# Performance work log

Hardware: AMD Instinct MI355X
Metric: run time of the kernel (lower is better)

The kernel has to match this reference:

```python
import jax, jax.numpy as jnp
import numpy as np

B, N, D = 4, 256, 256
NEG = -1e9


def setup_inputs() -> dict:
    key = jax.random.key(0)
    k = jax.random.split(key, 5)
    scale1 = 1.0 / np.sqrt(4 * D)
    scale2 = 1.0 / np.sqrt(D)
    return {
        "shared": jax.random.normal(k[0], (B, N, D), dtype=jnp.float32),
        "W1": jax.random.uniform(k[1], (4 * D, D), jnp.float32, -scale1, scale1),
        "b1": jax.random.uniform(k[2], (D,), jnp.float32, -scale1, scale1),
        "W2": jax.random.uniform(k[3], (D, 1), jnp.float32, -scale2, scale2),
        "b2": jax.random.uniform(k[4], (1,), jnp.float32, -scale2, scale2),
    }


def reference(shared, W1, b1, W2, b2):
    # Linear on concat([src, tgt, |src-tgt|, src*tgt]) == sum of per-block matmuls.
    Wa, Wb, Wc, Wd = W1[:D], W1[D:2 * D], W1[2 * D:3 * D], W1[3 * D:]
    src_t = jnp.einsum('bid,dh->bih', shared, Wa)        # [B,N,D]
    tgt_t = jnp.einsum('bjd,dh->bjh', shared, Wb)        # [B,N,D]
    diff = jnp.abs(shared[:, :, None, :] - shared[:, None, :, :])  # [B,N,N,D]
    prod = shared[:, :, None, :] * shared[:, None, :, :]           # [B,N,N,D]
    h = (src_t[:, :, None, :] + tgt_t[:, None, :, :]
         + jnp.einsum('bijd,dh->bijh', diff, Wc)
         + jnp.einsum('bijd,dh->bijh', prod, Wd) + b1)   # [B,N,N,D]
    h = jax.nn.silu(h)
    scores = jnp.einsum('bijh,h->bij', h, W2[:, 0]) + b2[0]  # [B,N,N]
    eye = jnp.eye(N, dtype=bool)[None]
    scores = jnp.where(eye, NEG, scores)
    return jax.nn.softmax(scores, axis=-1)
```

## Files before the change

kernel.cpp:

```cpp
#include <hip/hip_runtime.h>

#define BB 4
#define NN 256
#define DD 256
#define HH 256
#define NEGV -1.0e9f

typedef _Float16 half8 __attribute__((ext_vector_type(8)));
typedef __fp16   fp16x2 __attribute__((ext_vector_type(2)));
typedef float floatx4 __attribute__((ext_vector_type(4)));

__global__ __launch_bounds__(256) void prep_split(const float* __restrict__ X,
                                                  const float* __restrict__ W1,
                                                  float* __restrict__ S,
                                                  float* __restrict__ T,
                                                  _Float16* __restrict__ Wst) {
  const int g  = blockIdx.x;
  const int kk = blockIdx.y;
  const int h  = threadIdx.x;

  if (kk == 0 && g < 256) {
    const float wcv = W1[(size_t)(2 * DD + g) * HH + h];
    const float wdv = W1[(size_t)(3 * DD + g) * HH + h];
    const int ks = g >> 4;
    const int dd = g & 15;
    const int q  = dd >> 2;
    const int e  = (dd & 3) * 2;
    const int hgrp = h >> 4;
    const int ccw  = h & 15;
    _Float16* p = Wst + ((size_t)((ks * 16 + hgrp) * 4 + q) * 16 + ccw) * 8 + e;
    p[0] = (_Float16)wcv;
    p[1] = (_Float16)wdv;
  }

  const int row0 = g * 2;
  const int dbase = kk * 64;
  __shared__ float xr[2][64];
  if (h < 64)       xr[0][h]      = X[(size_t)row0 * DD + dbase + h];
  else if (h < 128) xr[1][h - 64] = X[(size_t)(row0 + 1) * DD + dbase + (h - 64)];
  __syncthreads();

  const float* __restrict__ Wa = W1 + (size_t)dbase * HH;
  const float* __restrict__ Wb = W1 + (size_t)(DD + dbase) * HH;
  float sa0 = 0.f, sa1 = 0.f, sb0 = 0.f, sb1 = 0.f;
#pragma unroll 8
  for (int d = 0; d < 64; ++d) {
    const float wa = Wa[(size_t)d * HH + h];
    const float wb = Wb[(size_t)d * HH + h];
    sa0 = fmaf(xr[0][d], wa, sa0);  sb0 = fmaf(xr[0][d], wb, sb0);
    sa1 = fmaf(xr[1][d], wa, sa1);  sb1 = fmaf(xr[1][d], wb, sb1);
  }
  atomicAdd(&S[(size_t)(row0 + 0) * HH + h], sa0);
  atomicAdd(&T[(size_t)(row0 + 0) * HH + h], sb0);
  atomicAdd(&S[(size_t)(row0 + 1) * HH + h], sa1);
  atomicAdd(&T[(size_t)(row0 + 1) * HH + h], sb1);
}

__device__ __forceinline__ half8 make_afrag(const float4 xi, const float4 xj) {
  fp16x2 p0 = __builtin_amdgcn_cvt_pkrtz(__builtin_fabsf(xi.x - xj.x), xi.x * xj.x);
  fp16x2 p1 = __builtin_amdgcn_cvt_pkrtz(__builtin_fabsf(xi.y - xj.y), xi.y * xj.y);
  fp16x2 p2 = __builtin_amdgcn_cvt_pkrtz(__builtin_fabsf(xi.z - xj.z), xi.z * xj.z);
  fp16x2 p3 = __builtin_amdgcn_cvt_pkrtz(__builtin_fabsf(xi.w - xj.w), xi.w * xj.w);
  uint4 u;
  u.x = __builtin_bit_cast(unsigned int, p0);
  u.y = __builtin_bit_cast(unsigned int, p1);
  u.z = __builtin_bit_cast(unsigned int, p2);
  u.w = __builtin_bit_cast(unsigned int, p3);
  return __builtin_bit_cast(half8, u);
}

#define MFMA16(af, bf, acc) acc = __builtin_amdgcn_mfma_f32_16x16x32_f16(af, bf, acc, 0, 0, 0)

__global__ __launch_bounds__(512, 4) void score_mfma(
    const float* __restrict__ X,  const float* __restrict__ b1,
    const float* __restrict__ W2, const float* __restrict__ b2,
    const float* __restrict__ S,  const float* __restrict__ T,
    const _Float16* __restrict__ Wst, float* __restrict__ Sc) {

  const int beta = blockIdx.x;
  const int b    = blockIdx.y;
  int i, qt;
  if (beta < 256)      { i = beta >> 2;                    qt = beta & 3; }
  else if (beta < 448) { const int g = beta - 256; const int d3 = g / 3;
                         i = 64 + d3;                      qt = 1 + (g - 3 * d3); }
  else if (beta < 576) { const int g = beta - 448;
                         i = 128 + (g >> 1);               qt = 2 + (g & 1); }
  else                 { i = 192 + (beta - 576);           qt = 3; }
  const int bi    = b * NN + i;
  const int jbase = qt * 64;
  const int isUp  = qt > (i >> 6);

  const int t     = threadIdx.x;
  const int lane  = t & 63;
  const int hg    = t >> 6;
  const int q     = lane >> 4;
  const int cc    = lane & 15;

  __shared__ __align__(16) float    xi_s[DD];
  __shared__ __align__(16) _Float16 Af[32768];
  __shared__ float pre_s[HH];
  __shared__ float pre2_s[HH];
  __shared__ float w2_s[HH];
  __shared__ float sc_s[8][64];

  if (t < 256) {
    xi_s[t]  = X[(size_t)bi * DD + t];
    pre_s[t] = S[(size_t)bi * HH + t] + b1[t];
  } else {
    const int u = t - 256;
    pre2_s[u] = T[(size_t)bi * HH + u] + b1[u];
    w2_s[u]   = W2[u];
  }

  const float* __restrict__ Tb = T + (size_t)b * NN * HH;
  const float* __restrict__ Sb = S + (size_t)b * NN * HH;

  const int jloc = t & 63;
  const int jg   = jloc >> 4;
  const int ccw  = jloc & 15;
  const float* __restrict__ xjrow = X + (size_t)(b * NN + jbase + jloc) * DD;

  const char* __restrict__ bsrc = (const char*)Wst + hg * 2048 + (size_t)lane * 16;

  __syncthreads();

  {
    const int sgrp = t >> 6;
#pragma unroll
    for (int idx = 0; idx < 8; ++idx) {
      const int ksqg = sgrp * 8 + idx;
      const int d0   = ksqg * 4;
      const int kg   = ksqg >> 2;
      const int qw   = ksqg & 3;
      const float4 xi4 = *(const float4*)&xi_s[d0];
      const float4 xj4 = *(const float4*)(xjrow + d0);
      *(half8*)&Af[kg * 2048 + (jg * 4 + qw) * 128 + ccw * 8] = make_afrag(xi4, xj4);
    }
  }
  __syncthreads();

  floatx4 acc0[4], acc1[4];
#pragma unroll
  for (int u = 0; u < 4; ++u) { acc0[u] = (floatx4)0.f; acc1[u] = (floatx4)0.f; }

  half8 Bf0[2], Bf1[2];
#pragma unroll
  for (int u = 0; u < 2; ++u) {
    Bf0[u] = *(const half8*)(bsrc + (size_t)u * 16384);
    Bf1[u] = *(const half8*)(bsrc + (size_t)u * 16384 + 1024);
  }
  const _Float16* ap0 = &Af[lane * 8];
  half8 An0 = *(const half8*)(ap0);
  half8 An1 = *(const half8*)(ap0 + 512);
  half8 An2 = *(const half8*)(ap0 + 1024);
  half8 An3 = *(const half8*)(ap0 + 1536);

#pragma unroll
  for (int kg = 0; kg < 16; ++kg) {
    const int s = kg & 1;
    const half8 Bc0 = Bf0[s], Bc1 = Bf1[s];
    const half8 Ac0 = An0, Ac1 = An1, Ac2 = An2, Ac3 = An3;
    if (kg < 14) {
      const char* bk = bsrc + (size_t)(kg + 2) * 16384;
      Bf0[s] = *(const half8*)(bk);
      Bf1[s] = *(const half8*)(bk + 1024);
    }
    if (kg < 15) {
      const _Float16* ap = &Af[(kg + 1) * 2048 + lane * 8];
      An0 = *(const half8*)(ap);
      An1 = *(const half8*)(ap + 512);
      An2 = *(const half8*)(ap + 1024);
      An3 = *(const half8*)(ap + 1536);
    }
    MFMA16(Ac0, Bc0, acc0[0]); MFMA16(Ac0, Bc1, acc1[0]);
    MFMA16(Ac1, Bc0, acc0[1]); MFMA16(Ac1, Bc1, acc1[1]);
    MFMA16(Ac2, Bc0, acc0[2]); MFMA16(Ac2, Bc1, acc1[2]);
    MFMA16(Ac3, Bc0, acc0[3]); MFMA16(Ac3, Bc1, acc1[3]);
  }

  const int h0   = hg * 32 + cc;
  const int h1   = h0 + 16;
  const int jrow = jbase + q * 4;

#define EPILOGUE(VROW, PRE) {                                                   \
    float tv0[16], tv1[16];                                                     \
    _Pragma("unroll")                                                           \
    for (int u = 0; u < 16; ++u) {                                              \
      const size_t j = (size_t)(jrow + (u >> 2) * 16 + (u & 3)) * HH;           \
      tv0[u] = VROW[j + h0];                                                    \
      tv1[u] = VROW[j + h1];                                                    \
    }                                                                           \
    const float w20 = w2_s[h0], pv0 = PRE[h0];                                  \
    const float w21 = w2_s[h1], pv1 = PRE[h1];                                  \
    float p[16];                                                                \
    _Pragma("unroll")                                                           \
    for (int u = 0; u < 16; ++u) {                                              \
      const float hv0 = acc0[u >> 2][u & 3] + pv0 + tv0[u];                     \
      const float sv0 = hv0 * __builtin_amdgcn_rcpf(1.f + __expf(-hv0));        \
      p[u] = sv0 * w20;                                                         \
      const float hv1 = acc1[u >> 2][u & 3] + pv1 + tv1[u];                     \
      const float sv1 = hv1 * __builtin_amdgcn_rcpf(1.f + __expf(-hv1));        \
      p[u] = fmaf(sv1, w21, p[u]);                                              \
    }                                                                           \
    _Pragma("unroll")                                                           \
    for (int u = 0; u < 16; ++u) {                                              \
      float v = p[u];                                                           \
      v += __shfl_xor(v, 1); v += __shfl_xor(v, 2);                             \
      v += __shfl_xor(v, 4); v += __shfl_xor(v, 8);                             \
      if (cc == 0) sc_s[hg][(u >> 2) * 16 + q * 4 + (u & 3)] = v;               \
    } }

  EPILOGUE(Tb, pre_s)
  __syncthreads();

  if (t < 64) {
    float s = sc_s[0][t] + sc_s[1][t] + sc_s[2][t] + sc_s[3][t]
            + sc_s[4][t] + sc_s[5][t] + sc_s[6][t] + sc_s[7][t] + b2[0];
    const int jg2 = jbase + t;
    if (jg2 == i) s = NEGV;
    Sc[(size_t)bi * NN + jg2] = s;
  }

  if (isUp) {
    __syncthreads();
    EPILOGUE(Sb, pre2_s)
    __syncthreads();
    if (t < 64) {
      const float s = sc_s[0][t] + sc_s[1][t] + sc_s[2][t] + sc_s[3][t]
                    + sc_s[4][t] + sc_s[5][t] + sc_s[6][t] + sc_s[7][t] + b2[0];
      Sc[(size_t)(b * NN + jbase + t) * NN + i] = s;
    }
  }
#undef EPILOGUE
}

__global__ __launch_bounds__(256) void softmax_kernel(const float* __restrict__ Sc,
                                                      float* __restrict__ out) {
  const int w    = threadIdx.x >> 6;
  const int lane = threadIdx.x & 63;
  const int bi   = blockIdx.x * 4 + w;
  const float4 v = *(const float4*)&Sc[(size_t)bi * NN + lane * 4];
  float m = fmaxf(fmaxf(v.x, v.y), fmaxf(v.z, v.w));
  m = fmaxf(m, __shfl_xor(m, 1));  m = fmaxf(m, __shfl_xor(m, 2));
  m = fmaxf(m, __shfl_xor(m, 4));  m = fmaxf(m, __shfl_xor(m, 8));
  m = fmaxf(m, __shfl_xor(m, 16)); m = fmaxf(m, __shfl_xor(m, 32));
  const float e0 = __expf(v.x - m), e1 = __expf(v.y - m);
  const float e2 = __expf(v.z - m), e3 = __expf(v.w - m);
  float sum = (e0 + e1) + (e2 + e3);
  sum += __shfl_xor(sum, 1);  sum += __shfl_xor(sum, 2);
  sum += __shfl_xor(sum, 4);  sum += __shfl_xor(sum, 8);
  sum += __shfl_xor(sum, 16); sum += __shfl_xor(sum, 32);
  const float r = 1.f / sum;
  float4 o; o.x = e0 * r; o.y = e1 * r; o.z = e2 * r; o.w = e3 * r;
  *(float4*)&out[(size_t)bi * NN + lane * 4] = o;
}

extern "C" void kernel_launch(void* const* d_in, const int* in_sizes, int n_in,
                              void* d_out, int out_size, void* d_ws, size_t ws_size,
                              hipStream_t stream) {
  const float* X  = (const float*)d_in[0];
  const float* W1 = (const float*)d_in[1];
  const float* b1 = (const float*)d_in[2];
  const float* W2 = (const float*)d_in[3];
  const float* b2 = (const float*)d_in[4];
  float* out = (float*)d_out;

  float*     Sws = (float*)d_ws;
  float*     Tws = Sws + (size_t)BB * NN * HH;
  _Float16*  Wst = (_Float16*)(Tws + (size_t)BB * NN * HH);
  float*     Scw = (float*)(Wst + (size_t)16 * HH * 32);

  hipMemsetAsync(Sws, 0, (size_t)2 * BB * NN * HH * sizeof(float), stream);

  prep_split<<<dim3(512, 4), 256, 0, stream>>>(X, W1, Sws, Tws, Wst);
  score_mfma<<<dim3(640, BB), 512, 0, stream>>>(X, b1, W2, b2, Sws, Tws, Wst, Scw);
  softmax_kernel<<<BB * NN / 4, 256, 0, stream>>>(Scw, out);
}
```

Baseline: 166.0 us.

## Process two query rows per block and drop atomic split-K in prep

The score kernel now handles two i rows per block, so each W-fragment global load feeds twice as many MFMAs and the xj row load is shared between both rows. The block count is halved, occupancy is lowered to 2 blocks per CU, and the A-fragment build is split into two k-halves to fit LDS. The prep kernel no longer splits K with atomics: each block does full 4-row dot products with float2 loads, which removes the memset and the atomic traffic. The cost is more registers (four accumulator sets), fewer resident waves, and an extra barrier pair per half.

```diff
diff --git a/kernel.cpp b/kernel.cpp
--- a/kernel.cpp
+++ b/kernel.cpp
@@ -10,50 +10,59 @@
 typedef __fp16   fp16x2 __attribute__((ext_vector_type(2)));
 typedef float floatx4 __attribute__((ext_vector_type(4)));
 
-__global__ __launch_bounds__(256) void prep_split(const float* __restrict__ X,
-                                                  const float* __restrict__ W1,
-                                                  float* __restrict__ S,
-                                                  float* __restrict__ T,
-                                                  _Float16* __restrict__ Wst) {
-  const int g  = blockIdx.x;
-  const int kk = blockIdx.y;
-  const int h  = threadIdx.x;
-
-  if (kk == 0 && g < 256) {
-    const float wcv = W1[(size_t)(2 * DD + g) * HH + h];
-    const float wdv = W1[(size_t)(3 * DD + g) * HH + h];
+__global__ __launch_bounds__(256) void prep(const float* __restrict__ X,
+                                            const float* __restrict__ W1,
+                                            float* __restrict__ S,
+                                            float* __restrict__ T,
+                                            _Float16* __restrict__ Wst) {
+  const int g = blockIdx.x;
+  const int t = threadIdx.x;
+
+  {
+    const float wcv = W1[(size_t)(2 * DD + g) * HH + t];
+    const float wdv = W1[(size_t)(3 * DD + g) * HH + t];
     const int ks = g >> 4;
     const int dd = g & 15;
     const int q  = dd >> 2;
     const int e  = (dd & 3) * 2;
-    const int hgrp = h >> 4;
-    const int ccw  = h & 15;
+    const int hgrp = t >> 4;
+    const int ccw  = t & 15;
     _Float16* p = Wst + ((size_t)((ks * 16 + hgrp) * 4 + q) * 16 + ccw) * 8 + e;
     p[0] = (_Float16)wcv;
     p[1] = (_Float16)wdv;
   }
 
-  const int row0 = g * 2;
-  const int dbase = kk * 64;
-  __shared__ float xr[2][64];
-  if (h < 64)       xr[0][h]      = X[(size_t)row0 * DD + dbase + h];
-  else if (h < 128) xr[1][h - 64] = X[(size_t)(row0 + 1) * DD + dbase + (h - 64)];
+  const int row0 = g * 4;
+  __shared__ float xr[4][256];
+  {
+    const float2* src2 = (const float2*)(X + (size_t)row0 * DD);
+    float2* xr2 = (float2*)xr;
+    xr2[t]       = src2[t];
+    xr2[t + 256] = src2[t + 256];
+  }
   __syncthreads();
 
-  const float* __restrict__ Wa = W1 + (size_t)dbase * HH;
-  const float* __restrict__ Wb = W1 + (size_t)(DD + dbase) * HH;
-  float sa0 = 0.f, sa1 = 0.f, sb0 = 0.f, sb1 = 0.f;
-#pragma unroll 8
-  for (int d = 0; d < 64; ++d) {
-    const float wa = Wa[(size_t)d * HH + h];
-    const float wb = Wb[(size_t)d * HH + h];
-    sa0 = fmaf(xr[0][d], wa, sa0);  sb0 = fmaf(xr[0][d], wb, sb0);
-    sa1 = fmaf(xr[1][d], wa, sa1);  sb1 = fmaf(xr[1][d], wb, sb1);
-  }
-  atomicAdd(&S[(size_t)(row0 + 0) * HH + h], sa0);
-  atomicAdd(&T[(size_t)(row0 + 0) * HH + h], sb0);
-  atomicAdd(&S[(size_t)(row0 + 1) * HH + h], sa1);
-  atomicAdd(&T[(size_t)(row0 + 1) * HH + h], sb1);
+  const int r2 = t >> 7;
+  const int h  = (t & 127) * 2;
+  const float* __restrict__ xA = xr[r2 * 2];
+  const float* __restrict__ xB = xr[r2 * 2 + 1];
+  float saAx = 0.f, saAy = 0.f, sbAx = 0.f, sbAy = 0.f;
+  float saBx = 0.f, saBy = 0.f, sbBx = 0.f, sbBy = 0.f;
+#pragma unroll 16
+  for (int d = 0; d < 256; ++d) {
+    const float2 wa = *(const float2*)&W1[(size_t)d * HH + h];
+    const float2 wb = *(const float2*)&W1[(size_t)(DD + d) * HH + h];
+    const float a = xA[d], c = xB[d];
+    saAx = fmaf(a, wa.x, saAx); saAy = fmaf(a, wa.y, saAy);
+    sbAx = fmaf(a, wb.x, sbAx); sbAy = fmaf(a, wb.y, sbAy);
+    saBx = fmaf(c, wa.x, saBx); saBy = fmaf(c, wa.y, saBy);
+    sbBx = fmaf(c, wb.x, sbBx); sbBy = fmaf(c, wb.y, sbBy);
+  }
+  const int rA = row0 + r2 * 2, rB = rA + 1;
+  *(float2*)&S[(size_t)rA * HH + h] = make_float2(saAx, saAy);
+  *(float2*)&S[(size_t)rB * HH + h] = make_float2(saBx, saBy);
+  *(float2*)&T[(size_t)rA * HH + h] = make_float2(sbAx, sbAy);
+  *(float2*)&T[(size_t)rB * HH + h] = make_float2(sbBx, sbBy);
 }
 
 __device__ __forceinline__ half8 make_afrag(const float4 xi, const float4 xj) {
@@ -71,7 +80,7 @@
 
 #define MFMA16(af, bf, acc) acc = __builtin_amdgcn_mfma_f32_16x16x32_f16(af, bf, acc, 0, 0, 0)
 
-__global__ __launch_bounds__(512, 4) void score_mfma(
+__global__ __launch_bounds__(512, 2) void score_mfma(
     const float* __restrict__ X,  const float* __restrict__ b1,
     const float* __restrict__ W2, const float* __restrict__ b2,
     const float* __restrict__ S,  const float* __restrict__ T,
@@ -79,16 +88,17 @@
 
   const int beta = blockIdx.x;
   const int b    = blockIdx.y;
-  int i, qt;
-  if (beta < 256)      { i = beta >> 2;                    qt = beta & 3; }
-  else if (beta < 448) { const int g = beta - 256; const int d3 = g / 3;
-                         i = 64 + d3;                      qt = 1 + (g - 3 * d3); }
-  else if (beta < 576) { const int g = beta - 448;
-                         i = 128 + (g >> 1);               qt = 2 + (g & 1); }
-  else                 { i = 192 + (beta - 576);           qt = 3; }
-  const int bi    = b * NN + i;
+  int m, qt;
+  if (beta < 128)      { m = beta >> 2;                    qt = beta & 3; }
+  else if (beta < 224) { const int g = beta - 128; const int d3 = g / 3;
+                         m = 32 + d3;                      qt = 1 + (g - 3 * d3); }
+  else if (beta < 288) { const int g = beta - 224;
+                         m = 64 + (g >> 1);                qt = 2 + (g & 1); }
+  else                 { m = 96 + (beta - 288);            qt = 3; }
+  const int i0    = m * 2;
+  const int bi0   = b * NN + i0;
   const int jbase = qt * 64;
-  const int isUp  = qt > (i >> 6);
+  const int isUp  = qt > (m >> 5);
 
   const int t     = threadIdx.x;
   const int lane  = t & 63;
@@ -96,20 +106,19 @@
   const int q     = lane >> 4;
   const int cc    = lane & 15;
 
-  __shared__ __align__(16) float    xi_s[DD];
-  __shared__ __align__(16) _Float16 Af[32768];
-  __shared__ float pre_s[HH];
-  __shared__ float pre2_s[HH];
+  __shared__ __align__(16) float    xi_s[2][DD];
+  __shared__ __align__(16) _Float16 Af[2][16384];
+  __shared__ float pre_s[2][HH];
+  __shared__ float pre2_s[2][HH];
   __shared__ float w2_s[HH];
-  __shared__ float sc_s[8][64];
-
-  if (t < 256) {
-    xi_s[t]  = X[(size_t)bi * DD + t];
-    pre_s[t] = S[(size_t)bi * HH + t] + b1[t];
-  } else {
-    const int u = t - 256;
-    pre2_s[u] = T[(size_t)bi * HH + u] + b1[u];
-    w2_s[u]   = W2[u];
+  __shared__ float sc_s[2][8][64];
+
+  {
+    const int ii = t >> 8, u = t & 255;
+    xi_s[ii][u]   = X[(size_t)(bi0 + ii) * DD + u];
+    pre_s[ii][u]  = S[(size_t)(bi0 + ii) * HH + u] + b1[u];
+    pre2_s[ii][u] = T[(size_t)(bi0 + ii) * HH + u] + b1[u];
+    if (t < 256) w2_s[t] = W2[t];
   }
 
   const float* __restrict__ Tb = T + (size_t)b * NN * HH;
@@ -122,26 +131,12 @@
 
   const char* __restrict__ bsrc = (const char*)Wst + hg * 2048 + (size_t)lane * 16;
 
-  __syncthreads();
-
-  {
-    const int sgrp = t >> 6;
+  floatx4 acc00[4], acc01[4], acc10[4], acc11[4];
 #pragma unroll
-    for (int idx = 0; idx < 8; ++idx) {
-      const int ksqg = sgrp * 8 + idx;
-      const int d0   = ksqg * 4;
-      const int kg   = ksqg >> 2;
-      const int qw   = ksqg & 3;
-      const float4 xi4 = *(const float4*)&xi_s[d0];
-      const float4 xj4 = *(const float4*)(xjrow + d0);
-      *(half8*)&Af[kg * 2048 + (jg * 4 + qw) * 128 + ccw * 8] = make_afrag(xi4, xj4);
-    }
-  }
-  __syncthreads();
-
-  floatx4 acc0[4], acc1[4];
-#pragma unroll
-  for (int u = 0; u < 4; ++u) { acc0[u] = (floatx4)0.f; acc1[u] = (floatx4)0.f; }
+  for (int u = 0; u < 4; ++u) {
+    acc00[u] = (floatx4)0.f; acc01[u] = (floatx4)0.f;
+    acc10[u] = (floatx4)0.f; acc11[u] = (floatx4)0.f;
+  }
 
   half8 Bf0[2], Bf1[2];
 #pragma unroll
@@ -149,33 +144,53 @@
     Bf0[u] = *(const half8*)(bsrc + (size_t)u * 16384);
     Bf1[u] = *(const half8*)(bsrc + (size_t)u * 16384 + 1024);
   }
-  const _Float16* ap0 = &Af[lane * 8];
-  half8 An0 = *(const half8*)(ap0);
-  half8 An1 = *(const half8*)(ap0 + 512);
-  half8 An2 = *(const half8*)(ap0 + 1024);
-  half8 An3 = *(const half8*)(ap0 + 1536);
+
+#pragma unroll 1
+  for (int half = 0; half < 2; ++half) {
+    __syncthreads();
 
 #pragma unroll
-  for (int kg = 0; kg < 16; ++kg) {
-    const int s = kg & 1;
-    const half8 Bc0 = Bf0[s], Bc1 = Bf1[s];
-    const half8 Ac0 = An0, Ac1 = An1, Ac2 = An2, Ac3 = An3;
-    if (kg < 14) {
-      const char* bk = bsrc + (size_t)(kg + 2) * 16384;
-      Bf0[s] = *(const half8*)(bk);
-      Bf1[s] = *(const half8*)(bk + 1024);
+    for (int idx = 0; idx < 4; ++idx) {
+      const int ksq = hg * 4 + idx;
+      const int d0  = (half * 32 + ksq) * 4;
+      const float4 xj4 = *(const float4*)(xjrow + d0);
+      const float4 xa4 = *(const float4*)&xi_s[0][d0];
+      const float4 xb4 = *(const float4*)&xi_s[1][d0];
+      const int off = (hg * 16 + jg * 4 + idx) * 128 + ccw * 8;
+      *(half8*)&Af[0][off] = make_afrag(xa4, xj4);
+      *(half8*)&Af[1][off] = make_afrag(xb4, xj4);
     }
-    if (kg < 15) {
-      const _Float16* ap = &Af[(kg + 1) * 2048 + lane * 8];
-      An0 = *(const half8*)(ap);
-      An1 = *(const half8*)(ap + 512);
-      An2 = *(const half8*)(ap + 1024);
-      An3 = *(const half8*)(ap + 1536);
+    __syncthreads();
+
+#pragma unroll
+    for (int ksl = 0; ksl < 8; ++ksl) {
+      const int s = ksl & 1;
+      const half8 Bc0 = Bf0[s], Bc1 = Bf1[s];
+      {
+        const int kn = (half * 8 + ksl + 2) & 15;
+        const char* bk = bsrc + (size_t)kn * 16384;
+        Bf0[s] = *(const half8*)(bk);
+        Bf1[s] = *(const half8*)(bk + 1024);
+      }
+      const _Float16* apA = &Af[0][ksl * 2048 + lane * 8];
+      const _Float16* apB = &Af[1][ksl * 2048 + lane * 8];
+      const half8 A00 = *(const half8*)(apA);
+      const half8 A01 = *(const half8*)(apA + 512);
+      const half8 A02 = *(const half8*)(apA + 1024);
+      const half8 A03 = *(const half8*)(apA + 1536);
+      const half8 A10 = *(const half8*)(apB);
+      const half8 A11 = *(const half8*)(apB + 512);
+      const half8 A12 = *(const half8*)(apB + 1024);
+      const half8 A13 = *(const half8*)(apB + 1536);
+      MFMA16(A00, Bc0, acc00[0]); MFMA16(A00, Bc1, acc01[0]);
+      MFMA16(A01, Bc0, acc00[1]); MFMA16(A01, Bc1, acc01[1]);
+      MFMA16(A02, Bc0, acc00[2]); MFMA16(A02, Bc1, acc01[2]);
+      MFMA16(A03, Bc0, acc00[3]); MFMA16(A03, Bc1, acc01[3]);
+      MFMA16(A10, Bc0, acc10[0]); MFMA16(A10, Bc1, acc11[0]);
+      MFMA16(A11, Bc0, acc10[1]); MFMA16(A11, Bc1, acc11[1]);
+      MFMA16(A12, Bc0, acc10[2]); MFMA16(A12, Bc1, acc11[2]);
+      MFMA16(A13, Bc0, acc10[3]); MFMA16(A13, Bc1, acc11[3]);
     }
-    MFMA16(Ac0, Bc0, acc0[0]); MFMA16(Ac0, Bc1, acc1[0]);
-    MFMA16(Ac1, Bc0, acc0[1]); MFMA16(Ac1, Bc1, acc1[1]);
-    MFMA16(Ac2, Bc0, acc0[2]); MFMA16(Ac2, Bc1, acc1[2]);
-    MFMA16(Ac3, Bc0, acc0[3]); MFMA16(Ac3, Bc1, acc1[3]);
   }
 
   const int h0   = hg * 32 + cc;
@@ -186,49 +201,66 @@
     float tv0[16], tv1[16];                                                     \
     _Pragma("unroll")                                                           \
     for (int u = 0; u < 16; ++u) {                                              \
-      const size_t j = (size_t)(jrow + (u >> 2) * 16 + (u & 3)) * HH;           \
-      tv0[u] = VROW[j + h0];                                                    \
-      tv1[u] = VROW[j + h1];                                                    \
+      const size_t jb = (size_t)(jrow + (u >> 2) * 16 + (u & 3)) * HH;          \
+      tv0[u] = VROW[jb + h0];                                                   \
+      tv1[u] = VROW[jb + h1];                                                   \
     }                                                                           \
-    const float w20 = w2_s[h0], pv0 = PRE[h0];                                  \
-    const float w21 = w2_s[h1], pv1 = PRE[h1];                                  \
-    float p[16];                                                                \
+    const float w20 = w2_s[h0], w21 = w2_s[h1];                                 \
+    const float pA0 = PRE[0][h0], pA1 = PRE[0][h1];                             \
+    const float pB0 = PRE[1][h0], pB1 = PRE[1][h1];                             \
+    float pI[16], pJ[16];                                                       \
     _Pragma("unroll")                                                           \
     for (int u = 0; u < 16; ++u) {                                              \
-      const float hv0 = acc0[u >> 2][u & 3] + pv0 + tv0[u];                     \
-      const float sv0 = hv0 * __builtin_amdgcn_rcpf(1.f + __expf(-hv0));        \
-      p[u] = sv0 * w20;                                                         \
-      const float hv1 = acc1[u >> 2][u & 3] + pv1 + tv1[u];                     \
-      const float sv1 = hv1 * __builtin_amdgcn_rcpf(1.f + __expf(-hv1));        \
-      p[u] = fmaf(sv1, w21, p[u]);                                              \
+      float hv, sv;                                                             \
+      hv = acc00[u >> 2][u & 3] + pA0 + tv0[u];                                 \
+      sv = hv * __builtin_amdgcn_rcpf(1.f + __expf(-hv));                       \
+      pI[u] = sv * w20;                                                         \
+      hv = acc01[u >> 2][u & 3] + pA1 + tv1[u];                                 \
+      sv = hv * __builtin_amdgcn_rcpf(1.f + __expf(-hv));                       \
+      pI[u] = fmaf(sv, w21, pI[u]);                                             \
+      hv = acc10[u >> 2][u & 3] + pB0 + tv0[u];                                 \
+      sv = hv * __builtin_amdgcn_rcpf(1.f + __expf(-hv));                       \
+      pJ[u] = sv * w20;                                                         \
+      hv = acc11[u >> 2][u & 3] + pB1 + tv1[u];                                 \
+      sv = hv * __builtin_amdgcn_rcpf(1.f + __expf(-hv));                       \
+      pJ[u] = fmaf(sv, w21, pJ[u]);                                             \
     }                                                                           \
     _Pragma("unroll")                                                           \
     for (int u = 0; u < 16; ++u) {                                              \
-      float v = p[u];                                                           \
+      float v = pI[u];                                                          \
       v += __shfl_xor(v, 1); v += __shfl_xor(v, 2);                             \
       v += __shfl_xor(v, 4); v += __shfl_xor(v, 8);                             \
-      if (cc == 0) sc_s[hg][(u >> 2) * 16 + q * 4 + (u & 3)] = v;               \
+      if (cc == 0) sc_s[0][hg][(u >> 2) * 16 + q * 4 + (u & 3)] = v;            \
+      float w = pJ[u];                                                          \
+      w += __shfl_xor(w, 1); w += __shfl_xor(w, 2);                             \
+      w += __shfl_xor(w, 4); w += __shfl_xor(w, 8);                             \
+      if (cc == 0) sc_s[1][hg][(u >> 2) * 16 + q * 4 + (u & 3)] = w;            \
     } }
 
   EPILOGUE(Tb, pre_s)
   __syncthreads();
 
-  if (t < 64) {
-    float s = sc_s[0][t] + sc_s[1][t] + sc_s[2][t] + sc_s[3][t]
-            + sc_s[4][t] + sc_s[5][t] + sc_s[6][t] + sc_s[7][t] + b2[0];
-    const int jg2 = jbase + t;
-    if (jg2 == i) s = NEGV;
-    Sc[(size_t)bi * NN + jg2] = s;
+  if (t < 128) {
+    const int r = t >> 6, jj = t & 63;
+    float s = sc_s[r][0][jj] + sc_s[r][1][jj] + sc_s[r][2][jj] + sc_s[r][3][jj]
+            + sc_s[r][4][jj] + sc_s[r][5][jj] + sc_s[r][6][jj] + sc_s[r][7][jj]
+            + b2[0];
+    const int jg2 = jbase + jj;
+    const int ii  = i0 + r;
+    if (jg2 == ii) s = NEGV;
+    Sc[(size_t)(b * NN + ii) * NN + jg2] = s;
   }
 
   if (isUp) {
     __syncthreads();
     EPILOGUE(Sb, pre2_s)
     __syncthreads();
-    if (t < 64) {
-      const float s = sc_s[0][t] + sc_s[1][t] + sc_s[2][t] + sc_s[3][t]
-                    + sc_s[4][t] + sc_s[5][t] + sc_s[6][t] + sc_s[7][t] + b2[0];
-      Sc[(size_t)(b * NN + jbase + t) * NN + i] = s;
+    if (t < 128) {
+      const int r = t >> 6, jj = t & 63;
+      const float s = sc_s[r][0][jj] + sc_s[r][1][jj] + sc_s[r][2][jj] + sc_s[r][3][jj]
+                    + sc_s[r][4][jj] + sc_s[r][5][jj] + sc_s[r][6][jj] + sc_s[r][7][jj]
+                    + b2[0];
+      Sc[(size_t)(b * NN + jbase + jj) * NN + (i0 + r)] = s;
     }
   }
 #undef EPILOGUE
@@ -270,9 +302,7 @@
   _Float16*  Wst = (_Float16*)(Tws + (size_t)BB * NN * HH);
   float*     Scw = (float*)(Wst + (size_t)16 * HH * 32);
 
-  hipMemsetAsync(Sws, 0, (size_t)2 * BB * NN * HH * sizeof(float), stream);
-
-  prep_split<<<dim3(512, 4), 256, 0, stream>>>(X, W1, Sws, Tws, Wst);
-  score_mfma<<<dim3(640, BB), 512, 0, stream>>>(X, b1, W2, b2, Sws, Tws, Wst, Scw);
+  prep<<<256, 256, 0, stream>>>(X, W1, Sws, Tws, Wst);
+  score_mfma<<<dim3(320, BB), 512, 0, stream>>>(X, b1, W2, b2, Sws, Tws, Wst, Scw);
   softmax_kernel<<<BB * NN / 4, 256, 0, stream>>>(Scw, out);
 }
```

After: 196.5 us. 1.18x slower.

## Drop split-K atomics in prep, deepen B prefetch, reorder score block mapping

Applied to the files above, without the earlier changes.

The prep kernel now computes each S/T row over the full D range with plain stores, which removes the memset and the atomicAdd split-K, and processes four rows per block with float2 weight loads. The score kernel's B-fragment prefetch goes from a depth of two to four and is issued before the A-fragment build barrier. The block index to (i, tile) mapping is regrouped by column tile. The gains are fewer launches and less atomic traffic plus more latency hiding, at the cost of fewer prep blocks and more registers in the score kernel.

```diff
diff --git a/kernel.cpp b/kernel.cpp
--- a/kernel.cpp
+++ b/kernel.cpp
@@ -10,50 +10,59 @@
 typedef __fp16   fp16x2 __attribute__((ext_vector_type(2)));
 typedef float floatx4 __attribute__((ext_vector_type(4)));
 
-__global__ __launch_bounds__(256) void prep_split(const float* __restrict__ X,
-                                                  const float* __restrict__ W1,
-                                                  float* __restrict__ S,
-                                                  float* __restrict__ T,
-                                                  _Float16* __restrict__ Wst) {
-  const int g  = blockIdx.x;
-  const int kk = blockIdx.y;
-  const int h  = threadIdx.x;
-
-  if (kk == 0 && g < 256) {
-    const float wcv = W1[(size_t)(2 * DD + g) * HH + h];
-    const float wdv = W1[(size_t)(3 * DD + g) * HH + h];
+__global__ __launch_bounds__(256) void prep(const float* __restrict__ X,
+                                            const float* __restrict__ W1,
+                                            float* __restrict__ S,
+                                            float* __restrict__ T,
+                                            _Float16* __restrict__ Wst) {
+  const int g = blockIdx.x;
+  const int t = threadIdx.x;
+
+  {
+    const float wcv = W1[(size_t)(2 * DD + g) * HH + t];
+    const float wdv = W1[(size_t)(3 * DD + g) * HH + t];
     const int ks = g >> 4;
     const int dd = g & 15;
     const int q  = dd >> 2;
     const int e  = (dd & 3) * 2;
-    const int hgrp = h >> 4;
-    const int ccw  = h & 15;
+    const int hgrp = t >> 4;
+    const int ccw  = t & 15;
     _Float16* p = Wst + ((size_t)((ks * 16 + hgrp) * 4 + q) * 16 + ccw) * 8 + e;
     p[0] = (_Float16)wcv;
     p[1] = (_Float16)wdv;
   }
 
-  const int row0 = g * 2;
-  const int dbase = kk * 64;
-  __shared__ float xr[2][64];
-  if (h < 64)       xr[0][h]      = X[(size_t)row0 * DD + dbase + h];
-  else if (h < 128) xr[1][h - 64] = X[(size_t)(row0 + 1) * DD + dbase + (h - 64)];
-  __syncthreads();
-
-  const float* __restrict__ Wa = W1 + (size_t)dbase * HH;
-  const float* __restrict__ Wb = W1 + (size_t)(DD + dbase) * HH;
-  float sa0 = 0.f, sa1 = 0.f, sb0 = 0.f, sb1 = 0.f;
-#pragma unroll 8
-  for (int d = 0; d < 64; ++d) {
-    const float wa = Wa[(size_t)d * HH + h];
-    const float wb = Wb[(size_t)d * HH + h];
-    sa0 = fmaf(xr[0][d], wa, sa0);  sb0 = fmaf(xr[0][d], wb, sb0);
-    sa1 = fmaf(xr[1][d], wa, sa1);  sb1 = fmaf(xr[1][d], wb, sb1);
-  }
-  atomicAdd(&S[(size_t)(row0 + 0) * HH + h], sa0);
-  atomicAdd(&T[(size_t)(row0 + 0) * HH + h], sb0);
-  atomicAdd(&S[(size_t)(row0 + 1) * HH + h], sa1);
-  atomicAdd(&T[(size_t)(row0 + 1) * HH + h], sb1);
+  const int row0 = g * 4;
+  __shared__ float xr[4][256];
+  {
+    const float2* src2 = (const float2*)(X + (size_t)row0 * DD);
+    float2* xr2 = (float2*)xr;
+    xr2[t]       = src2[t];
+    xr2[t + 256] = src2[t + 256];
+  }
+  __syncthreads();
+
+  const int r2 = t >> 7;
+  const int h  = (t & 127) * 2;
+  const float* __restrict__ xA = xr[r2 * 2];
+  const float* __restrict__ xB = xr[r2 * 2 + 1];
+  float saAx = 0.f, saAy = 0.f, sbAx = 0.f, sbAy = 0.f;
+  float saBx = 0.f, saBy = 0.f, sbBx = 0.f, sbBy = 0.f;
+#pragma unroll 16
+  for (int d = 0; d < 256; ++d) {
+    const float2 wa = *(const float2*)&W1[(size_t)d * HH + h];
+    const float2 wb = *(const float2*)&W1[(size_t)(DD + d) * HH + h];
+    const float a = xA[d], c = xB[d];
+    saAx = fmaf(a, wa.x, saAx); saAy = fmaf(a, wa.y, saAy);
+    sbAx = fmaf(a, wb.x, sbAx); sbAy = fmaf(a, wb.y, sbAy);
+    saBx = fmaf(c, wa.x, saBx); saBy = fmaf(c, wa.y, saBy);
+    sbBx = fmaf(c, wb.x, sbBx); sbBy = fmaf(c, wb.y, sbBy);
+  }
+  const int rA = row0 + r2 * 2, rB = rA + 1;
+  *(float2*)&S[(size_t)rA * HH + h] = make_float2(saAx, saAy);
+  *(float2*)&S[(size_t)rB * HH + h] = make_float2(saBx, saBy);
+  *(float2*)&T[(size_t)rA * HH + h] = make_float2(sbAx, sbAy);
+  *(float2*)&T[(size_t)rB * HH + h] = make_float2(sbBx, sbBy);
 }
 
 __device__ __forceinline__ half8 make_afrag(const float4 xi, const float4 xj) {
@@ -80,12 +89,10 @@
   const int beta = blockIdx.x;
   const int b    = blockIdx.y;
   int i, qt;
-  if (beta < 256)      { i = beta >> 2;                    qt = beta & 3; }
-  else if (beta < 448) { const int g = beta - 256; const int d3 = g / 3;
-                         i = 64 + d3;                      qt = 1 + (g - 3 * d3); }
-  else if (beta < 576) { const int g = beta - 448;
-                         i = 128 + (g >> 1);               qt = 2 + (g & 1); }
-  else                 { i = 192 + (beta - 576);           qt = 3; }
+  if (beta < 64)       { qt = 0; i = beta; }
+  else if (beta < 192) { qt = 1; i = beta - 64; }
+  else if (beta < 384) { qt = 2; i = beta - 192; }
+  else                 { qt = 3; i = beta - 384; }
   const int bi    = b * NN + i;
   const int jbase = qt * 64;
   const int isUp  = qt > (i >> 6);
@@ -121,6 +128,13 @@
   const float* __restrict__ xjrow = X + (size_t)(b * NN + jbase + jloc) * DD;
 
   const char* __restrict__ bsrc = (const char*)Wst + hg * 2048 + (size_t)lane * 16;
+
+  half8 Bf0[4], Bf1[4];
+#pragma unroll
+  for (int u = 0; u < 4; ++u) {
+    Bf0[u] = *(const half8*)(bsrc + (size_t)u * 16384);
+    Bf1[u] = *(const half8*)(bsrc + (size_t)u * 16384 + 1024);
+  }
 
   __syncthreads();
 
@@ -143,12 +157,6 @@
 #pragma unroll
   for (int u = 0; u < 4; ++u) { acc0[u] = (floatx4)0.f; acc1[u] = (floatx4)0.f; }
 
-  half8 Bf0[2], Bf1[2];
-#pragma unroll
-  for (int u = 0; u < 2; ++u) {
-    Bf0[u] = *(const half8*)(bsrc + (size_t)u * 16384);
-    Bf1[u] = *(const half8*)(bsrc + (size_t)u * 16384 + 1024);
-  }
   const _Float16* ap0 = &Af[lane * 8];
   half8 An0 = *(const half8*)(ap0);
   half8 An1 = *(const half8*)(ap0 + 512);
@@ -157,11 +165,11 @@
 
 #pragma unroll
   for (int kg = 0; kg < 16; ++kg) {
-    const int s = kg & 1;
+    const int s = kg & 3;
     const half8 Bc0 = Bf0[s], Bc1 = Bf1[s];
     const half8 Ac0 = An0, Ac1 = An1, Ac2 = An2, Ac3 = An3;
-    if (kg < 14) {
-      const char* bk = bsrc + (size_t)(kg + 2) * 16384;
+    if (kg < 12) {
+      const char* bk = bsrc + (size_t)(kg + 4) * 16384;
       Bf0[s] = *(const half8*)(bk);
       Bf1[s] = *(const half8*)(bk + 1024);
     }
@@ -270,9 +278,7 @@
   _Float16*  Wst = (_Float16*)(Tws + (size_t)BB * NN * HH);
   float*     Scw = (float*)(Wst + (size_t)16 * HH * 32);
 
-  hipMemsetAsync(Sws, 0, (size_t)2 * BB * NN * HH * sizeof(float), stream);
-
-  prep_split<<<dim3(512, 4), 256, 0, stream>>>(X, W1, Sws, Tws, Wst);
+  prep<<<256, 256, 0, stream>>>(X, W1, Sws, Tws, Wst);
   score_mfma<<<dim3(640, BB), 512, 0, stream>>>(X, b1, W2, b2, Sws, Tws, Wst, Scw);
   softmax_kernel<<<BB * NN / 4, 256, 0, stream>>>(Scw, out);
 }
```

New measurement: 162.8 us. Within noise of the previous version (-1.9%).
